# Kernel tuning notes

Measured on AMD Instinct MI355X. Metric: run time of the kernel, lower is better.

The kernel has to match this reference:

```python
import jax, jax.numpy as jnp
import numpy as np

B, S, D = 4, 2048, 1024

def setup_inputs() -> dict:
    key = jax.random.key(0)
    k1, k2, k3, k4 = jax.random.split(key, 4)
    scale = 1.0 / np.sqrt(D)
    token_encodings = jax.random.normal(k1, (B, S, D), dtype=jnp.float32)
    W_q = jax.random.normal(k2, (D, D), dtype=jnp.float32) * scale
    W_k = jax.random.normal(k3, (D, D), dtype=jnp.float32) * scale
    W_v = jax.random.normal(k4, (D, D), dtype=jnp.float32) * scale
    # causal mask, broadcastable to (B, S, S); 0 means masked
    mask = jnp.tril(jnp.ones((S, S), dtype=jnp.int32))[None, :, :]
    return {"token_encodings": token_encodings, "mask": mask,
            "W_q": W_q, "W_k": W_k, "W_v": W_v}

def reference(token_encodings, mask, W_q, W_k, W_v):
    # nn.Linear(d, d, bias=False): y = x @ W.T
    q = jnp.einsum('bsd,ed->bse', token_encodings, W_q)
    k = jnp.einsum('bsd,ed->bse', token_encodings, W_k)
    v = jnp.einsum('bsd,ed->bse', token_encodings, W_v)
    d_k = q.shape[-1]
    scores = jnp.einsum('bqd,bkd->bqk', q, k) / jnp.sqrt(jnp.asarray(d_k, q.dtype))
    scores = jnp.where(mask == 0, jnp.asarray(-jnp.inf, scores.dtype), scores)
    attn_weights = jax.nn.softmax(scores, axis=-1)
    output = jnp.einsum('bqk,bkd->bqd', attn_weights, v)
    return (output, attn_weights)
```

## Files before the change

### kernel.cpp

```cpp
#include <hip/hip_runtime.h>
#include <hip/hip_bf16.h>
#include <stdint.h>
#include <math.h>


typedef __hip_bfloat16 bf16;
typedef __attribute__((ext_vector_type(8))) short short8;
typedef __attribute__((ext_vector_type(4))) float f32x4;

#define BM 128
#define BN 128
#define BK 32

static constexpr int Bb = 4;
static constexpr int S  = 2048;
static constexpr int D  = 1024;
static constexpr size_t QK_ELEMS = (size_t)Bb * S * D;
static constexpr size_t SS_ELEMS = (size_t)S * S;
static constexpr size_t W_ELEMS  = (size_t)D * D;

__device__ __forceinline__ void async16(const bf16* g, bf16* l) {
  __builtin_amdgcn_global_load_lds(
      (__attribute__((address_space(1))) const void*)g,
      (__attribute__((address_space(3))) void*)l, 16, 0, 0);
}

template<bool SWAP>
__device__ __forceinline__ void gemm_core(const bf16* __restrict__ A,
                                          const bf16* __restrict__ B,
                                          int ldA, int ldB, int ksteps,
                                          bf16* As, bf16* Bs,
                                          f32x4 acc[4][4])
{
  const int tid  = threadIdx.x;
  const int lane = tid & 63;
  const int wave = tid >> 6;
  const int wm   = (wave & 1) * 64;
  const int wn   = (wave >> 1) * 64;
  const int m16  = lane & 15;
  const int kq   = lane >> 4;

  const int c0 = tid,        c1 = tid + 256;
  const int r0 = c0 >> 2;    const int f0 = (c0 & 3) * 8;
  const int r1 = c1 >> 2;    const int f1 = (c1 & 3) * 8;

  for (int ks = 0; ks < ksteps; ++ks) {
    const int k = ks * BK;
    async16(A + (size_t)r0 * ldA + k + f0, As + (size_t)c0 * 8);
    async16(A + (size_t)r1 * ldA + k + f1, As + (size_t)c1 * 8);
    async16(B + (size_t)r0 * ldB + k + f0, Bs + (size_t)c0 * 8);
    async16(B + (size_t)r1 * ldB + k + f1, Bs + (size_t)c1 * 8);
    __syncthreads();

    short8 af[4], bfrag[4];
    #pragma unroll
    for (int i = 0; i < 4; ++i)
      af[i] = *(const short8*)&As[(wm + i * 16 + m16) * BK + kq * 8];
    #pragma unroll
    for (int i = 0; i < 4; ++i)
      bfrag[i] = *(const short8*)&Bs[(wn + i * 16 + m16) * BK + kq * 8];

    #pragma unroll
    for (int mi = 0; mi < 4; ++mi) {
      #pragma unroll
      for (int ni = 0; ni < 4; ++ni) {
        if (SWAP)
          acc[mi][ni] = __builtin_amdgcn_mfma_f32_16x16x32_bf16(
              bfrag[ni], af[mi], acc[mi][ni], 0, 0, 0);
        else
          acc[mi][ni] = __builtin_amdgcn_mfma_f32_16x16x32_bf16(
              af[mi], bfrag[ni], acc[mi][ni], 0, 0, 0);
      }
    }
    __syncthreads();
  }
}

__device__ __forceinline__ void zero_acc(f32x4 acc[4][4]) {
  #pragma unroll
  for (int mi = 0; mi < 4; ++mi)
    #pragma unroll
    for (int ni = 0; ni < 4; ++ni)
      acc[mi][ni] = (f32x4){0.f, 0.f, 0.f, 0.f};
}

__device__ __forceinline__ unsigned short f2b(float f) {
  __hip_bfloat16 h = __float2bfloat16(f);
  return *(unsigned short*)&h;
}

__global__ __launch_bounds__(256)
void cvt_kernel(const float* __restrict__ X,  const float* __restrict__ Wq,
                const float* __restrict__ Wk, const float* __restrict__ Wv,
                bf16* __restrict__ Xb, bf16* __restrict__ Wqb,
                bf16* __restrict__ Wkb, bf16* __restrict__ Wvb)
{
  const size_t g = ((size_t)blockIdx.x * 256 + threadIdx.x) * 4;
  const float* src; bf16* dst; size_t off;
  if (g < QK_ELEMS) { src = X; dst = Xb; off = g; }
  else {
    const size_t h = g - QK_ELEMS;
    const int w = (int)(h >> 20);
    off = h & (W_ELEMS - 1);
    src = (w == 0) ? Wq : (w == 1) ? Wk : Wv;
    dst = (w == 0) ? Wqb : (w == 1) ? Wkb : Wvb;
  }
  const float4 v = *(const float4*)(src + off);
  uint2 o;
  o.x = (uint32_t)f2b(v.x) | ((uint32_t)f2b(v.y) << 16);
  o.y = (uint32_t)f2b(v.z) | ((uint32_t)f2b(v.w) << 16);
  *(uint2*)((unsigned short*)dst + off) = o;
}

__global__ __launch_bounds__(256, 2)
void qk_kernel(const bf16* __restrict__ X, const bf16* __restrict__ Wq,
               const bf16* __restrict__ Wk, bf16* __restrict__ Q,
               bf16* __restrict__ Ko)
{
  __shared__ __align__(16) bf16 As[BM * BK];
  __shared__ __align__(16) bf16 Bs[BN * BK];
  const int nt = blockIdx.x, mt = blockIdx.y, z = blockIdx.z;
  const bf16* W = z ? Wk : Wq;
  bf16* Out = z ? Ko : Q;

  f32x4 acc[4][4];
  zero_acc(acc);
  gemm_core<false>(X + (size_t)mt * 128 * D, W + (size_t)nt * 128 * D,
                   D, D, D / BK, As, Bs, acc);

  const int lane = threadIdx.x & 63, wave = threadIdx.x >> 6;
  const int wm = (wave & 1) * 64, wn = (wave >> 1) * 64;
  const int col0 = lane & 15, row0 = (lane >> 4) * 4;
  #pragma unroll
  for (int mi = 0; mi < 4; ++mi)
    #pragma unroll
    for (int ni = 0; ni < 4; ++ni)
      #pragma unroll
      for (int r = 0; r < 4; ++r) {
        const int grow = mt * 128 + wm + mi * 16 + row0 + r;
        const int gcol = nt * 128 + wn + ni * 16 + col0;
        Out[(size_t)grow * D + gcol] = __float2bfloat16(acc[mi][ni][r]);
      }
}

__global__ __launch_bounds__(256, 2)
void vt_kernel(const bf16* __restrict__ X, const bf16* __restrict__ Wv,
               bf16* __restrict__ Vt)
{
  __shared__ __align__(16) bf16 As[BM * BK];
  __shared__ __align__(16) bf16 Bs[BN * BK];
  const int nt = blockIdx.x, mt = blockIdx.y;

  f32x4 acc[4][4];
  zero_acc(acc);
  gemm_core<true>(X + (size_t)mt * 128 * D, Wv + (size_t)nt * 128 * D,
                  D, D, D / BK, As, Bs, acc);

  const int lane = threadIdx.x & 63, wave = threadIdx.x >> 6;
  const int wm = (wave & 1) * 64, wn = (wave >> 1) * 64;
  const int col0 = lane & 15, row0 = (lane >> 4) * 4;
  const int b = (mt * 128) >> 11;
  #pragma unroll
  for (int mi = 0; mi < 4; ++mi)
    #pragma unroll
    for (int ni = 0; ni < 4; ++ni)
      #pragma unroll
      for (int r = 0; r < 4; ++r) {
        const int ge = nt * 128 + wn + ni * 16 + row0 + r;
        const int gs = mt * 128 + wm + mi * 16 + col0;
        const int sl = gs & (S - 1);
        Vt[(size_t)b * D * S + (size_t)ge * S + sl] = __float2bfloat16(acc[mi][ni][r]);
      }
}

__global__ __launch_bounds__(256, 2)
void scores_kernel(const bf16* __restrict__ Q, const bf16* __restrict__ K,
                   float* __restrict__ Sc)
{
  const int kt = blockIdx.x, qt = blockIdx.y, b = blockIdx.z;
  if (kt > qt) return;
  __shared__ __align__(16) bf16 As[BM * BK];
  __shared__ __align__(16) bf16 Bs[BN * BK];

  f32x4 acc[4][4];
  zero_acc(acc);
  gemm_core<false>(Q + ((size_t)b * S + qt * 128) * D,
                   K + ((size_t)b * S + kt * 128) * D,
                   D, D, D / BK, As, Bs, acc);

  const int lane = threadIdx.x & 63, wave = threadIdx.x >> 6;
  const int wm = (wave & 1) * 64, wn = (wave >> 1) * 64;
  const int col0 = lane & 15, row0 = (lane >> 4) * 4;
  float* out = Sc + (size_t)b * SS_ELEMS;
  #pragma unroll
  for (int mi = 0; mi < 4; ++mi)
    #pragma unroll
    for (int ni = 0; ni < 4; ++ni)
      #pragma unroll
      for (int r = 0; r < 4; ++r) {
        const int gq = qt * 128 + wm + mi * 16 + row0 + r;
        const int gk = kt * 128 + wn + ni * 16 + col0;
        out[(size_t)gq * S + gk] = acc[mi][ni][r] * 0.03125f;
      }
}

__device__ __forceinline__ float wave_max(float v) {
  #pragma unroll
  for (int o = 32; o > 0; o >>= 1) v = fmaxf(v, __shfl_xor(v, o, 64));
  return v;
}
__device__ __forceinline__ float wave_sum(float v) {
  #pragma unroll
  for (int o = 32; o > 0; o >>= 1) v += __shfl_xor(v, o, 64);
  return v;
}

__global__ __launch_bounds__(256)
void softmax_kernel(float* __restrict__ Attn, bf16* __restrict__ Pb)
{
  const int row = blockIdx.x;
  const int b = row >> 11, i = row & (S - 1);
  float* s = Attn + (size_t)b * SS_ELEMS + (size_t)i * S;
  bf16* p  = Pb   + (size_t)b * SS_ELEMS + (size_t)i * S;
  const int t = threadIdx.x;
  const int lane = t & 63, wave = t >> 6;
  __shared__ float red[4];

  float vals[8];
  #pragma unroll
  for (int u = 0; u < 8; ++u) {
    const int j = t + u * 256;
    vals[u] = (j <= i) ? s[j] : -INFINITY;
  }
  float m = -INFINITY;
  #pragma unroll
  for (int u = 0; u < 8; ++u) m = fmaxf(m, vals[u]);
  m = wave_max(m);
  if (lane == 0) red[wave] = m;
  __syncthreads();
  m = fmaxf(fmaxf(red[0], red[1]), fmaxf(red[2], red[3]));
  __syncthreads();

  float sum = 0.f;
  #pragma unroll
  for (int u = 0; u < 8; ++u) {
    const float e = expf(vals[u] - m);
    vals[u] = e;
    sum += e;
  }
  sum = wave_sum(sum);
  if (lane == 0) red[wave] = sum;
  __syncthreads();
  sum = red[0] + red[1] + red[2] + red[3];
  const float inv = 1.f / sum;

  #pragma unroll
  for (int u = 0; u < 8; ++u) {
    const int j = t + u * 256;
    const float w = vals[u] * inv;
    s[j] = w;
    p[j] = __float2bfloat16(w);
  }
}

__global__ __launch_bounds__(256, 2)
void out_kernel(const bf16* __restrict__ P, const bf16* __restrict__ Vt,
                float* __restrict__ O)
{
  const int dt = blockIdx.x, qt = blockIdx.y, b = blockIdx.z;
  __shared__ __align__(16) bf16 As[BM * BK];
  __shared__ __align__(16) bf16 Bs[BN * BK];

  f32x4 acc[4][4];
  zero_acc(acc);
  const int ksteps = (qt + 1) * (128 / BK);
  gemm_core<false>(P + (size_t)b * SS_ELEMS + (size_t)qt * 128 * S,
                   Vt + (size_t)b * D * S + (size_t)dt * 128 * S,
                   S, S, ksteps, As, Bs, acc);

  const int lane = threadIdx.x & 63, wave = threadIdx.x >> 6;
  const int wm = (wave & 1) * 64, wn = (wave >> 1) * 64;
  const int col0 = lane & 15, row0 = (lane >> 4) * 4;
  #pragma unroll
  for (int mi = 0; mi < 4; ++mi)
    #pragma unroll
    for (int ni = 0; ni < 4; ++ni)
      #pragma unroll
      for (int r = 0; r < 4; ++r) {
        const int gq = qt * 128 + wm + mi * 16 + row0 + r;
        const int gd = dt * 128 + wn + ni * 16 + col0;
        O[((size_t)b * S + gq) * D + gd] = acc[mi][ni][r];
      }
}

extern "C" void kernel_launch(void* const* d_in, const int* in_sizes, int n_in,
                              void* d_out, int out_size, void* d_ws, size_t ws_size,
                              hipStream_t stream) {
  const float* X  = (const float*)d_in[0];
  const float* Wq = (const float*)d_in[2];
  const float* Wk = (const float*)d_in[3];
  const float* Wv = (const float*)d_in[4];

  float* Out  = (float*)d_out;
  float* Attn = Out + QK_ELEMS;

  bf16* Q   = (bf16*)d_ws;
  bf16* K   = Q + QK_ELEMS;
  bf16* Vt  = K + QK_ELEMS;
  bf16* Xb  = Vt + QK_ELEMS;
  bf16* Wqb = Xb + QK_ELEMS;
  bf16* Wkb = Wqb + W_ELEMS;
  bf16* Wvb = Wkb + W_ELEMS;
  bf16* Pb  = (bf16*)d_ws;

  const int cvt_blocks = (int)((QK_ELEMS + 3 * W_ELEMS) / 4 / 256);
  cvt_kernel<<<cvt_blocks, 256, 0, stream>>>(X, Wq, Wk, Wv, Xb, Wqb, Wkb, Wvb);
  qk_kernel<<<dim3(D / 128, (Bb * S) / 128, 2), 256, 0, stream>>>(Xb, Wqb, Wkb, Q, K);
  vt_kernel<<<dim3(D / 128, (Bb * S) / 128, 1), 256, 0, stream>>>(Xb, Wvb, Vt);
  scores_kernel<<<dim3(S / 128, S / 128, Bb), 256, 0, stream>>>(Q, K, Attn);
  softmax_kernel<<<dim3(Bb * S), 256, 0, stream>>>(Attn, Pb);
  out_kernel<<<dim3(D / 128, S / 128, Bb), 256, 0, stream>>>(Pb, Vt, Out);
}
```

Before: 320.9 us.

## Merge QKV projections, launch only causal score tiles, reorder out tiles

Combines the Q/K and V projection GEMMs into one launch with a third grid slice, so the V tiles share the wave with Q/K and the tail of one launch no longer idles. The scores kernel now launches only the lower-triangular tiles and maps the linear block index to (qt,kt) with a sqrt-based inverse, which removes the empty early-exit blocks. The out kernel processes the heaviest query tiles first, which should balance the tail. Launch bounds are raised to 3 blocks per CU, which may force register spills.

```diff
diff --git a/kernel.cpp b/kernel.cpp
--- a/kernel.cpp
+++ b/kernel.cpp
@@ -112,73 +112,65 @@
   *(uint2*)((unsigned short*)dst + off) = o;
 }
 
-__global__ __launch_bounds__(256, 2)
-void qk_kernel(const bf16* __restrict__ X, const bf16* __restrict__ Wq,
-               const bf16* __restrict__ Wk, bf16* __restrict__ Q,
-               bf16* __restrict__ Ko)
+__global__ __launch_bounds__(256, 3)
+void qkv_kernel(const bf16* __restrict__ X, const bf16* __restrict__ Wq,
+                const bf16* __restrict__ Wk, const bf16* __restrict__ Wv,
+                bf16* __restrict__ Q, bf16* __restrict__ Ko,
+                bf16* __restrict__ Vt)
 {
   __shared__ __align__(16) bf16 As[BM * BK];
   __shared__ __align__(16) bf16 Bs[BN * BK];
   const int nt = blockIdx.x, mt = blockIdx.y, z = blockIdx.z;
-  const bf16* W = z ? Wk : Wq;
-  bf16* Out = z ? Ko : Q;
-
-  f32x4 acc[4][4];
-  zero_acc(acc);
-  gemm_core<false>(X + (size_t)mt * 128 * D, W + (size_t)nt * 128 * D,
-                   D, D, D / BK, As, Bs, acc);
+  const bf16* W = (z == 0) ? Wq : (z == 1) ? Wk : Wv;
 
   const int lane = threadIdx.x & 63, wave = threadIdx.x >> 6;
   const int wm = (wave & 1) * 64, wn = (wave >> 1) * 64;
   const int col0 = lane & 15, row0 = (lane >> 4) * 4;
-  #pragma unroll
-  for (int mi = 0; mi < 4; ++mi)
-    #pragma unroll
-    for (int ni = 0; ni < 4; ++ni)
-      #pragma unroll
-      for (int r = 0; r < 4; ++r) {
-        const int grow = mt * 128 + wm + mi * 16 + row0 + r;
-        const int gcol = nt * 128 + wn + ni * 16 + col0;
-        Out[(size_t)grow * D + gcol] = __float2bfloat16(acc[mi][ni][r]);
-      }
-}
-
-__global__ __launch_bounds__(256, 2)
-void vt_kernel(const bf16* __restrict__ X, const bf16* __restrict__ Wv,
-               bf16* __restrict__ Vt)
-{
-  __shared__ __align__(16) bf16 As[BM * BK];
-  __shared__ __align__(16) bf16 Bs[BN * BK];
-  const int nt = blockIdx.x, mt = blockIdx.y;
 
   f32x4 acc[4][4];
   zero_acc(acc);
-  gemm_core<true>(X + (size_t)mt * 128 * D, Wv + (size_t)nt * 128 * D,
-                  D, D, D / BK, As, Bs, acc);
-
-  const int lane = threadIdx.x & 63, wave = threadIdx.x >> 6;
-  const int wm = (wave & 1) * 64, wn = (wave >> 1) * 64;
-  const int col0 = lane & 15, row0 = (lane >> 4) * 4;
-  const int b = (mt * 128) >> 11;
-  #pragma unroll
-  for (int mi = 0; mi < 4; ++mi)
-    #pragma unroll
-    for (int ni = 0; ni < 4; ++ni)
-      #pragma unroll
-      for (int r = 0; r < 4; ++r) {
-        const int ge = nt * 128 + wn + ni * 16 + row0 + r;
-        const int gs = mt * 128 + wm + mi * 16 + col0;
-        const int sl = gs & (S - 1);
-        Vt[(size_t)b * D * S + (size_t)ge * S + sl] = __float2bfloat16(acc[mi][ni][r]);
-      }
-}
-
-__global__ __launch_bounds__(256, 2)
+  if (z < 2) {
+    gemm_core<false>(X + (size_t)mt * 128 * D, W + (size_t)nt * 128 * D,
+                     D, D, D / BK, As, Bs, acc);
+    bf16* Out = z ? Ko : Q;
+    #pragma unroll
+    for (int mi = 0; mi < 4; ++mi)
+      #pragma unroll
+      for (int ni = 0; ni < 4; ++ni)
+        #pragma unroll
+        for (int r = 0; r < 4; ++r) {
+          const int grow = mt * 128 + wm + mi * 16 + row0 + r;
+          const int gcol = nt * 128 + wn + ni * 16 + col0;
+          Out[(size_t)grow * D + gcol] = __float2bfloat16(acc[mi][ni][r]);
+        }
+  } else {
+    gemm_core<true>(X + (size_t)mt * 128 * D, W + (size_t)nt * 128 * D,
+                    D, D, D / BK, As, Bs, acc);
+    const int b = (mt * 128) >> 11;
+    #pragma unroll
+    for (int mi = 0; mi < 4; ++mi)
+      #pragma unroll
+      for (int ni = 0; ni < 4; ++ni)
+        #pragma unroll
+        for (int r = 0; r < 4; ++r) {
+          const int ge = nt * 128 + wn + ni * 16 + row0 + r;
+          const int gs = mt * 128 + wm + mi * 16 + col0;
+          const int sl = gs & (S - 1);
+          Vt[(size_t)b * D * S + (size_t)ge * S + sl] = __float2bfloat16(acc[mi][ni][r]);
+        }
+  }
+}
+
+__global__ __launch_bounds__(256, 3)
 void scores_kernel(const bf16* __restrict__ Q, const bf16* __restrict__ K,
                    float* __restrict__ Sc)
 {
-  const int kt = blockIdx.x, qt = blockIdx.y, b = blockIdx.z;
-  if (kt > qt) return;
+  const int t = blockIdx.x, b = blockIdx.y;
+  int qt = (int)((sqrtf(8.f * (float)t + 1.f) - 1.f) * 0.5f);
+  while ((qt + 1) * (qt + 2) / 2 <= t) ++qt;
+  while (qt * (qt + 1) / 2 > t) --qt;
+  const int kt = t - qt * (qt + 1) / 2;
+
   __shared__ __align__(16) bf16 As[BM * BK];
   __shared__ __align__(16) bf16 Bs[BN * BK];
 
@@ -263,11 +255,11 @@
   }
 }
 
-__global__ __launch_bounds__(256, 2)
+__global__ __launch_bounds__(256, 3)
 void out_kernel(const bf16* __restrict__ P, const bf16* __restrict__ Vt,
                 float* __restrict__ O)
 {
-  const int dt = blockIdx.x, qt = blockIdx.y, b = blockIdx.z;
+  const int dt = blockIdx.x, qt = (S / 128 - 1) - blockIdx.y, b = blockIdx.z;
   __shared__ __align__(16) bf16 As[BM * BK];
   __shared__ __align__(16) bf16 Bs[BN * BK];
 
@@ -315,9 +307,10 @@
 
   const int cvt_blocks = (int)((QK_ELEMS + 3 * W_ELEMS) / 4 / 256);
   cvt_kernel<<<cvt_blocks, 256, 0, stream>>>(X, Wq, Wk, Wv, Xb, Wqb, Wkb, Wvb);
-  qk_kernel<<<dim3(D / 128, (Bb * S) / 128, 2), 256, 0, stream>>>(Xb, Wqb, Wkb, Q, K);
-  vt_kernel<<<dim3(D / 128, (Bb * S) / 128, 1), 256, 0, stream>>>(Xb, Wvb, Vt);
-  scores_kernel<<<dim3(S / 128, S / 128, Bb), 256, 0, stream>>>(Q, K, Attn);
+  qkv_kernel<<<dim3(D / 128, (Bb * S) / 128, 3), 256, 0, stream>>>(
+      Xb, Wqb, Wkb, Wvb, Q, K, Vt);
+  const int ntile = (S / 128) * (S / 128 + 1) / 2;
+  scores_kernel<<<dim3(ntile, Bb), 256, 0, stream>>>(Q, K, Attn);
   softmax_kernel<<<dim3(Bb * S), 256, 0, stream>>>(Attn, Pb);
   out_kernel<<<dim3(D / 128, S / 128, Bb), 256, 0, stream>>>(Pb, Vt, Out);
 }
```

Result: no change. 315.7 us (-1.6%).
